# Kernel tuning notes

Measured on AMD Instinct MI355X. Metric: run time of the kernel, lower is better.

## Reference

```python
import itertools
import jax, jax.numpy as jnp
import numpy as np

B, S, D = 256, 49, 448          # batch, tokens (7x7), channels
H, KD, ED = 8, 32, 128          # heads, key_dim, expanded_key_dim (attn_ratio*key_dim)
QKV_OUT = H * (KD + KD + ED)    # 1536
MLP_HID = 4 * D                 # 1792
EPS = 1e-12
SCALE = KD ** -0.5


def _bias_idxs(resolution=7):
    points = list(itertools.product(range(resolution), range(resolution)))
    offsets, idxs = {}, []
    for p1 in points:
        for p2 in points:
            off = (abs(p1[0] - p2[0]), abs(p1[1] - p2[1]))
            if off not in offsets:
                offsets[off] = len(offsets)
            idxs.append(offsets[off])
    n = len(points)
    return np.asarray(idxs, np.int32).reshape(n, n), len(offsets)


def setup_inputs() -> dict:
    key = jax.random.key(0)
    ks = jax.random.split(key, 12)
    idxs_np, n_off = _bias_idxs(7)  # [49,49], 49 offsets
    s = 0.02
    return {
        "hidden_states": jax.random.normal(ks[0], (B, S, D), jnp.float32),
        "ln2_w": jnp.ones((D,), jnp.float32),
        "ln2_b": jnp.zeros((D,), jnp.float32),
        "qkv_w": jax.random.normal(ks[1], (QKV_OUT, D), jnp.float32) * s,
        "qkv_b": jnp.zeros((QKV_OUT,), jnp.float32),
        "proj_w": jax.random.normal(ks[2], (D, H * ED), jnp.float32) * s,
        "proj_b": jnp.zeros((D,), jnp.float32),
        "attention_biases": jax.random.normal(ks[3], (H, n_off), jnp.float32) * s,
        "fc1_w": jax.random.normal(ks[4], (MLP_HID, D), jnp.float32) * s,
        "fc1_b": jnp.zeros((MLP_HID,), jnp.float32),
        "fc2_w": jax.random.normal(ks[5], (D, MLP_HID), jnp.float32) * s,
        "fc2_b": jnp.zeros((D,), jnp.float32),
        "layer_scale_1": jnp.full((D,), 1e-5, jnp.float32),
        "layer_scale_2": jnp.full((D,), 1e-5, jnp.float32),
        "attention_bias_idxs": jnp.asarray(idxs_np),  # int32 [49,49]
    }


def _layernorm(x, w, b):
    mu = jnp.mean(x, axis=-1, keepdims=True)
    var = jnp.mean(jnp.square(x - mu), axis=-1, keepdims=True)
    return (x - mu) * jax.lax.rsqrt(var + EPS) * w + b


def reference(hidden_states, ln2_w, ln2_b, qkv_w, qkv_b, proj_w, proj_b,
              attention_biases, fc1_w, fc1_b, fc2_w, fc2_b,
              layer_scale_1, layer_scale_2, attention_bias_idxs):
    # NOTE: upstream code applies norm2 before BOTH attention and MLP (faithful).
    norm = _layernorm(hidden_states, ln2_w, ln2_b)  # [B,S,D]

    qkv = (norm @ qkv_w.T + qkv_b).reshape(B, S, H, KD + KD + ED)
    q, k, v = jnp.split(qkv, [KD, 2 * KD], axis=-1)  # [B,S,H,KD/KD/ED]

    bias = attention_biases[:, attention_bias_idxs]  # [H,S,S] gathered rel-pos bias
    scores = jnp.einsum("bqhd,bkhd->bhqk", q, k) * SCALE + bias[None]
    probs = jax.nn.softmax(scores, axis=-1)          # [B,H,S,S]

    ctx = jnp.einsum("bhqk,bkhd->bqhd", probs, v).reshape(B, S, H * ED)
    attn_out = ctx @ proj_w.T + proj_b               # [B,S,D]

    out = hidden_states + layer_scale_1 * attn_out
    mlp = jax.nn.gelu(norm @ fc1_w.T + fc1_b, approximate=False) @ fc2_w.T + fc2_b
    out = out + layer_scale_2 * mlp
    return out
```

## Files before the change

kernel.cpp:

```cpp
#include <hip/hip_runtime.h>
#include <hip/hip_bf16.h>
#include <cstdint>

#define B_    256
#define S_    49
#define D_    448
#define H_    8
#define NTOK  (B_*S_)
#define QKVO  1536
#define MLPH  1792
#define SCALE_ 0.17677669529663687f

using bf16x8  = __attribute__((ext_vector_type(8))) __bf16;
using ushort8 = __attribute__((ext_vector_type(8))) unsigned short;
using f32x4   = __attribute__((ext_vector_type(4))) float;

__device__ __forceinline__ unsigned short f2bf(float f){
  uint32_t u = __builtin_bit_cast(uint32_t, f);
  u += 0x7fffu + ((u >> 16) & 1u);
  return (unsigned short)(u >> 16);
}
__device__ __forceinline__ float b2f(unsigned short b){
  uint32_t u = ((uint32_t)b) << 16;
  return __builtin_bit_cast(float, u);
}

__device__ __forceinline__ void gload_lds16(const void* g, void* l){
  __builtin_amdgcn_global_load_lds(
      (const __attribute__((address_space(1))) void*)g,
      (__attribute__((address_space(3))) void*)l, 16, 0, 0);
}

#define P_S0 688128L
#define P_S1 1490944L
#define P_S2 1949696L
#define P_S3 2752512L
#define P_S4 2932736L
#define P_S5 2936064L
#define P_S6 2936576L
#define P_S7 2969344L
#define PREP_BLKS 6628
__global__ __launch_bounds__(448)
void prepln_k(const float* __restrict__ x, const float* __restrict__ lw,
              const float* __restrict__ lb, unsigned short* __restrict__ normb,
              const float* __restrict__ qkvw, const float* __restrict__ fc1w,
              const float* __restrict__ projw, const float* __restrict__ fc2w,
              const float* __restrict__ ls1, const float* __restrict__ ls2,
              const float* __restrict__ qkvb, const float* __restrict__ fc1b,
              const float* __restrict__ projb, const float* __restrict__ fc2b,
              const float* __restrict__ attb, const int* __restrict__ idxs,
              unsigned short* __restrict__ wcat, unsigned short* __restrict__ wfused,
              float* __restrict__ cbig, float* __restrict__ cbv,
              float* __restrict__ biasf){
  const int bid = blockIdx.x, t = threadIdx.x;
  if (bid < NTOK){
    const float v = x[(size_t)bid*448 + t];
    float s1 = v, s2 = v*v;
    #pragma unroll
    for (int o = 32; o; o >>= 1){ s1 += __shfl_xor(s1, o); s2 += __shfl_xor(s2, o); }
    __shared__ float a1[7], a2[7];
    const int wid = t >> 6;
    if ((t & 63) == 0){ a1[wid] = s1; a2[wid] = s2; }
    __syncthreads();
    float S1 = 0.f, S2 = 0.f;
    #pragma unroll
    for (int i = 0; i < 7; ++i){ S1 += a1[i]; S2 += a2[i]; }
    const float mu  = S1 * (1.f/448.f);
    const float var = S2 * (1.f/448.f) - mu*mu;
    const float rs  = rsqrtf(var + 1e-12f);
    normb[(size_t)bid*448 + t] = f2bf((v - mu)*rs*lw[t] + lb[t]);
  } else {
    const long i = (long)(bid - NTOK)*448 + t;
    if (i < P_S0){
      wcat[i] = f2bf(qkvw[i]);
    } else if (i < P_S1){
      long j = i - P_S0;
      wcat[i] = f2bf(fc1w[j]);
    } else if (i < P_S2){
      long j = i - P_S1;
      long r = j / 1024;
      wfused[r*2816 + (j - r*1024)] = f2bf(projw[j]*ls1[r]);
    } else if (i < P_S3){
      long j = i - P_S2;
      long r = j / 1792;
      wfused[r*2816 + 1024 + (j - r*1792)] = f2bf(fc2w[j]*ls2[r]);
    } else if (i < P_S4){
      long j = i - P_S3;
      wfused[448L*2816 + j] = 0;
    } else if (i < P_S5){
      long j = i - P_S4;
      cbig[j] = (j < 1536) ? qkvb[j] : fc1b[j - 1536];
    } else if (i < P_S6){
      long j = i - P_S5;
      cbv[j] = (j < 448) ? ls1[j]*projb[j] + ls2[j]*fc2b[j] : 0.f;
    } else if (i < P_S7){
      long j = i - P_S6;
      int h = (int)(j >> 12), r = (int)((j >> 6) & 63), c = (int)(j & 63);
      float v;
      if (c >= 49) v = -1e30f;
      else { int q = r < 49 ? r : 48; v = attb[h*49 + idxs[q*49 + c]]; }
      biasf[j] = v;
    }
  }
}

__global__ __launch_bounds__(256)
void gemm4_k(const unsigned short* __restrict__ A,
             const unsigned short* __restrict__ W,
             const float* __restrict__ bias,
             unsigned short* __restrict__ outB1,
             unsigned short* __restrict__ outB2,
             int splitBy, int nby)
{
  __shared__ char smem[65536];

  const int NB = gridDim.x;
  const int q8 = NB >> 3, r8 = NB & 7;
  const int xcd = blockIdx.x & 7, idx = blockIdx.x >> 3;
  const int wgid = (xcd < r8 ? xcd*(q8+1) : r8*(q8+1) + (xcd-r8)*q8) + idx;
  const int bx = wgid / nby, by = wgid - bx*nby;

  const int t = threadIdx.x, lane = t & 63, wid = t >> 6;
  const int wm = wid >> 1, wn = wid & 1;
  const int g = lane >> 4, li = lane & 15;
  f32x4 acc[4][4] = {};

  const int l3   = lane >> 3;
  const int sp   = (lane & 7) ^ l3;
  const int rofs = 2*l3 + (sp >> 2);
  const int cofs = (sp & 3)*8;

  auto stage = [&](int buf, int kt){
    char* Asb = smem + buf*16384;
    char* Bsb = Asb + 8192;
    const int k0 = kt*32;
    #pragma unroll
    for (int i = 0; i < 2; ++i){
      const int c = wid*2 + i;
      gload_lds16(A + (size_t)(bx*128 + c*16 + rofs)*448 + k0 + cofs, Asb + c*1024);
    }
    #pragma unroll
    for (int i = 0; i < 2; ++i){
      const int c = wid*2 + i;
      gload_lds16(W + (size_t)(by*128 + c*16 + rofs)*448 + k0 + cofs, Bsb + c*1024);
    }
  };

  const int sOff = (li >> 1)*128 + ((((li & 1)*4 + g) ^ (li >> 1)) << 4);

  stage(0, 0);
  stage(1, 1);
  int cur = 0, stg = 2;
  for (int kt = 0; kt < 14; ++kt){
    if (kt < 13) asm volatile("s_waitcnt vmcnt(4)" ::: "memory");
    else         asm volatile("s_waitcnt vmcnt(0)" ::: "memory");
    __builtin_amdgcn_s_barrier();
    if (kt + 2 < 14){ stage(stg, kt + 2); stg = (stg == 2) ? 0 : stg + 1; }
    char* Asb = smem + cur*16384;
    char* Bsb = Asb + 8192;
    bf16x8 af[4], bfr[4];
    #pragma unroll
    for (int mf = 0; mf < 4; ++mf)
      af[mf] = *reinterpret_cast<const bf16x8*>(Asb + (wm*4 + mf)*1024 + sOff);
    #pragma unroll
    for (int nf = 0; nf < 4; ++nf)
      bfr[nf] = *reinterpret_cast<const bf16x8*>(Bsb + (wn*4 + nf)*1024 + sOff);
    __builtin_amdgcn_s_setprio(1);
    #pragma unroll
    for (int mf = 0; mf < 4; ++mf)
      #pragma unroll
      for (int nf = 0; nf < 4; ++nf)
        acc[mf][nf] = __builtin_amdgcn_mfma_f32_16x16x32_bf16(af[mf], bfr[nf], acc[mf][nf], 0, 0, 0);
    __builtin_amdgcn_s_setprio(0);
    cur = (cur == 2) ? 0 : cur + 1;
  }
  __syncthreads();

  const bool dogelu = by >= splitBy;
  #pragma unroll
  for (int mf = 0; mf < 4; ++mf){
    #pragma unroll
    for (int nf = 0; nf < 4; ++nf){
      const int col = wn*64 + nf*16 + li;
      const float bi = bias[by*128 + col];
      #pragma unroll
      for (int j = 0; j < 4; ++j){
        const int row = wm*64 + mf*16 + g*4 + j;
        float v = acc[mf][nf][j] + bi;
        if (dogelu) v = 0.5f*v*(1.0f + erff(v*0.70710678118654752f));
        *reinterpret_cast<float*>(smem + row*512 + ((col*4) ^ (((row >> 2) & 3) << 6))) = v;
      }
    }
  }
  __syncthreads();
  const int lr = lane >> 4, lc = lane & 15;
  #pragma unroll
  for (int it = 0; it < 8; ++it){
    const int r = wid*32 + it*4 + lr;
    const int sw = ((r >> 2) & 3) << 6;
    const f32x4 v0 = *reinterpret_cast<const f32x4*>(smem + r*512 + ((lc*32)      ^ sw));
    const f32x4 v1 = *reinterpret_cast<const f32x4*>(smem + r*512 + ((lc*32 + 16) ^ sw));
    ushort8 u;
    #pragma unroll
    for (int k = 0; k < 4; ++k){ u[k] = f2bf(v0[k]); u[4+k] = f2bf(v1[k]); }
    const int grow = bx*128 + r;
    if (by < splitBy)
      *reinterpret_cast<ushort8*>(outB1 + (size_t)grow*QKVO + by*128 + lc*8) = u;
    else
      *reinterpret_cast<ushort8*>(outB2 + (size_t)grow*MLPH + (by - splitBy)*128 + lc*8) = u;
  }
}

__global__ __launch_bounds__(256)
void gemm1_k(const unsigned short* __restrict__ A1, int lda1, int nkt1,
             const unsigned short* __restrict__ A2, int lda2, int nkt,
             const unsigned short* __restrict__ W, int ldw,
             const float* __restrict__ bias,
             const float* __restrict__ resid, float* __restrict__ outF,
             int nby)
{
  constexpr int BN = 64, NF = 2;
  __shared__ char smem[49152];

  const int NB = gridDim.x;
  const int q8 = NB >> 3, r8 = NB & 7;
  const int xcd = blockIdx.x & 7, idx = blockIdx.x >> 3;
  const int wgid = (xcd < r8 ? xcd*(q8+1) : r8*(q8+1) + (xcd-r8)*q8) + idx;
  const int bx = wgid / nby, by = wgid - bx*nby;

  const int t = threadIdx.x, lane = t & 63, wid = t >> 6;
  const int wm = wid >> 1, wn = wid & 1;
  const int g = lane >> 4, li = lane & 15;
  f32x4 acc[4][NF] = {};

  const int srow  = lane >> 3;
  const int scolw = ((lane & 7) ^ srow) * 8;

  auto stage = [&](int buf, int kt){
    char* Asb = smem + buf*16384;
    char* Bsb = smem + 32768 + buf*(BN*128);
    const unsigned short* Ab; int lda, k0;
    if (kt < nkt1){ Ab = A1; lda = lda1; k0 = kt*64; }
    else          { Ab = A2; lda = lda2; k0 = (kt - nkt1)*64; }
    #pragma unroll
    for (int i = 0; i < 4; ++i){
      const int c = wid*4 + i;
      gload_lds16(Ab + (size_t)(bx*128 + c*8 + srow)*lda + k0 + scolw,
                  Asb + c*1024);
    }
    #pragma unroll
    for (int i = 0; i < NF; ++i){
      const int c = wid*NF + i;
      gload_lds16(W + (size_t)(by*BN + c*8 + srow)*ldw + kt*64 + scolw,
                  Bsb + c*1024);
    }
  };

  int buf = 0;
  stage(0, 0);
  for (int kt = 0; kt < nkt; ++kt){
    __syncthreads();
    if (kt + 1 < nkt) stage(buf ^ 1, kt + 1);
    char* Asb = smem + buf*16384;
    char* Bsb = smem + 32768 + buf*(BN*128);
    #pragma unroll
    for (int ks = 0; ks < 2; ++ks){
      const int kk2 = (ks*32 + g*8)*2;
      bf16x8 af[4], bfr[NF];
      #pragma unroll
      for (int mf = 0; mf < 4; ++mf){
        const int row = wm*64 + mf*16 + li;
        af[mf] = *reinterpret_cast<const bf16x8*>(
            Asb + row*128 + (kk2 ^ ((row & 7) << 4)));
      }
      #pragma unroll
      for (int nf = 0; nf < NF; ++nf){
        const int row = wn*(BN/2) + nf*16 + li;
        bfr[nf] = *reinterpret_cast<const bf16x8*>(
            Bsb + row*128 + (kk2 ^ ((row & 7) << 4)));
      }
      #pragma unroll
      for (int mf = 0; mf < 4; ++mf)
        #pragma unroll
        for (int nf = 0; nf < NF; ++nf)
          acc[mf][nf] = __builtin_amdgcn_mfma_f32_16x16x32_bf16(af[mf], bfr[nf], acc[mf][nf], 0, 0, 0);
    }
    buf ^= 1;
  }
  __syncthreads();

  const int lr = lane >> 4, lc = lane & 15;
  #pragma unroll
  for (int mf = 0; mf < 4; ++mf){
    #pragma unroll
    for (int nf = 0; nf < NF; ++nf){
      const int col = wn*32 + nf*16 + li;
      const float bi = bias[by*64 + col];
      #pragma unroll
      for (int j = 0; j < 4; ++j){
        const int rt = wm*64 + mf*16 + g*4 + j;
        *reinterpret_cast<float*>(smem + rt*256 + ((col*4) ^ (((rt >> 2) & 1) << 6)))
            = acc[mf][nf][j] + bi;
      }
    }
  }
  __syncthreads();
  #pragma unroll
  for (int i = 0; i < 8; ++i){
    const int r = wid*32 + i*4 + lr;
    const int sw = ((r >> 2) & 1) << 6;
    const f32x4 v = *reinterpret_cast<const f32x4*>(smem + r*256 + ((lc*16) ^ sw));
    const size_t o = (size_t)(bx*128 + r)*448 + by*64 + lc*4;
    const f32x4 rs = *reinterpret_cast<const f32x4*>(resid + o);
    *reinterpret_cast<f32x4*>(outF + o) = rs + v;
  }
}

__global__ __launch_bounds__(256)
void attn_mfma_k(const unsigned short* __restrict__ qkv,
                 const float* __restrict__ biasf,
                 unsigned short* __restrict__ ctx)
{
  const int bh = blockIdx.x;
  const int b = bh >> 3, h = bh & 7;
  __shared__ unsigned short QKs[64*64];
  __shared__ unsigned short Vs[64*128];
  __shared__ unsigned short Ps[64*64];
  const int t = threadIdx.x, lane = t & 63, w = t >> 6;
  const int g = lane >> 4, li = lane & 15;
  const size_t qbase = ((size_t)b*49)*QKVO + (size_t)h*192;

  {
    const int kk = lane >> 3, ss = lane & 7;
    #pragma unroll
    for (int i = 0; i < 2; ++i){
      const int kb = (w*2 + i)*8;
      const int k  = kb + kk;
      const int ks = k < 49 ? k : 48;
      gload_lds16(qkv + qbase + (size_t)ks*QKVO + ((ss ^ (k & 7))*8),
                  (char*)QKs + kb*128);
    }
    const int kv = lane >> 4, sv = lane & 15;
    #pragma unroll
    for (int i = 0; i < 4; ++i){
      const int kb = (w*4 + i)*4;
      const int k  = kb + kv;
      const int ks = k < 49 ? k : 48;
      const int swz = (((unsigned)k >> 3) & 3) << 1;
      gload_lds16(qkv + qbase + 64 + (size_t)ks*QKVO + ((sv ^ swz)*8),
                  (char*)Vs + kb*256);
    }
  }
  asm volatile("s_waitcnt vmcnt(0)" ::: "memory");
  for (int e = t; e < 15*8; e += 256){
    const int k = 49 + (e >> 3), s = e & 7;
    *reinterpret_cast<bf16x8*>((char*)QKs + k*128 + s*16) = (bf16x8){};
  }
  for (int e = t; e < 15*16; e += 256){
    const int k = 49 + (e >> 4), s = e & 15;
    *reinterpret_cast<bf16x8*>((char*)Vs + k*256 + s*16) = (bf16x8){};
  }
  __syncthreads();

  const int qrow = w*16 + li;
  const bf16x8 afq = *reinterpret_cast<const bf16x8*>(
      (char*)QKs + qrow*128 + ((g ^ (qrow & 7)) << 4));
  f32x4 accs[4];
  #pragma unroll
  for (int nf = 0; nf < 4; ++nf){
    const int krow = nf*16 + li;
    const bf16x8 bfr = *reinterpret_cast<const bf16x8*>(
        (char*)QKs + krow*128 + (((4 + g) ^ (krow & 7)) << 4));
    f32x4 z = {};
    accs[nf] = __builtin_amdgcn_mfma_f32_16x16x32_bf16(afq, bfr, z, 0, 0, 0);
  }

  #pragma unroll
  for (int j = 0; j < 4; ++j){
    const int row = w*16 + g*4 + j;
    float sv[4];
    #pragma unroll
    for (int nf = 0; nf < 4; ++nf)
      sv[nf] = accs[nf][j]*SCALE_ + biasf[h*4096 + row*64 + nf*16 + li];
    float m = fmaxf(fmaxf(sv[0], sv[1]), fmaxf(sv[2], sv[3]));
    #pragma unroll
    for (int o = 8; o; o >>= 1) m = fmaxf(m, __shfl_xor(m, o));
    float e[4], s = 0.f;
    #pragma unroll
    for (int nf = 0; nf < 4; ++nf){ e[nf] = __expf(sv[nf] - m); s += e[nf]; }
    #pragma unroll
    for (int o = 8; o; o >>= 1) s += __shfl_xor(s, o);
    const float inv = 1.f / s;
    #pragma unroll
    for (int nf = 0; nf < 4; ++nf){
      const int byte = (row*128 + (nf*16 + li)*2) ^ ((row & 7) << 4);
      *reinterpret_cast<unsigned short*>((char*)Ps + byte) = f2bf(e[nf]*inv);
    }
  }
  __syncthreads();

  f32x4 accp[4][2] = {};
  #pragma unroll
  for (int kt = 0; kt < 2; ++kt){
    bf16x8 pa[4];
    #pragma unroll
    for (int mt = 0; mt < 4; ++mt){
      const int q = mt*16 + li;
      const int byte = (q*128 + kt*64 + g*16) ^ ((q & 7) << 4);
      pa[mt] = *reinterpret_cast<const bf16x8*>((char*)Ps + byte);
    }
    #pragma unroll
    for (int nf = 0; nf < 2; ++nf){
      const int d = w*32 + nf*16 + li;
      ushort8 vbu;
      #pragma unroll
      for (int j = 0; j < 8; ++j){
        const int k = kt*32 + g*8 + j;
        const int byte = (k*256 + d*2) ^ ((((unsigned)k >> 3) & 3) << 5);
        vbu[j] = *reinterpret_cast<const unsigned short*>((char*)Vs + byte);
      }
      const bf16x8 vb = __builtin_bit_cast(bf16x8, vbu);
      #pragma unroll
      for (int mt = 0; mt < 4; ++mt)
        accp[mt][nf] = __builtin_amdgcn_mfma_f32_16x16x32_bf16(pa[mt], vb, accp[mt][nf], 0, 0, 0);
    }
  }

  const size_t obase = ((size_t)b*49)*1024 + (size_t)h*128;
  #pragma unroll
  for (int mt = 0; mt < 4; ++mt){
    #pragma unroll
    for (int nf = 0; nf < 2; ++nf){
      #pragma unroll
      for (int j = 0; j < 4; ++j){
        const int row = mt*16 + g*4 + j;
        if (row < 49){
          const int col = w*32 + nf*16 + li;
          ctx[obase + (size_t)row*1024 + col] = f2bf(accp[mt][nf][j]);
        }
      }
    }
  }
}

extern "C" void kernel_launch(void* const* d_in, const int* in_sizes, int n_in,
                              void* d_out, int out_size, void* d_ws, size_t ws_size,
                              hipStream_t stream)
{
  const float* hidden = (const float*)d_in[0];
  const float* ln2w   = (const float*)d_in[1];
  const float* ln2b   = (const float*)d_in[2];
  const float* qkvw   = (const float*)d_in[3];
  const float* qkvb   = (const float*)d_in[4];
  const float* projw  = (const float*)d_in[5];
  const float* projb  = (const float*)d_in[6];
  const float* attb   = (const float*)d_in[7];
  const float* fc1w   = (const float*)d_in[8];
  const float* fc1b   = (const float*)d_in[9];
  const float* fc2w   = (const float*)d_in[10];
  const float* fc2b   = (const float*)d_in[11];
  const float* ls1    = (const float*)d_in[12];
  const float* ls2    = (const float*)d_in[13];
  const int*   aidx   = (const int*)d_in[14];
  float* out = (float*)d_out;

  char* p = (char*)d_ws;
  auto alloc = [&](size_t bytes){ void* r = (void*)p; p += (bytes + 255) & ~(size_t)255; return r; };
  unsigned short* wcat   = (unsigned short*)alloc((size_t)3328*448*2);
  unsigned short* wfused = (unsigned short*)alloc((size_t)512*2816*2);
  unsigned short* normb  = (unsigned short*)alloc((size_t)NTOK*448*2);
  unsigned short* qkvv   = (unsigned short*)alloc((size_t)NTOK*QKVO*2);
  unsigned short* ctx    = (unsigned short*)alloc((size_t)NTOK*1024*2);
  unsigned short* hid    = (unsigned short*)alloc((size_t)NTOK*MLPH*2);
  float*          biasf  = (float*)alloc((size_t)8*64*64*4);
  float*          cbig   = (float*)alloc((size_t)3328*4);
  float*          cbv    = (float*)alloc((size_t)512*4);

  prepln_k<<<NTOK + PREP_BLKS, 448, 0, stream>>>(hidden, ln2w, ln2b, normb,
                                                 qkvw, fc1w, projw, fc2w, ls1, ls2,
                                                 qkvb, fc1b, projb, fc2b, attb, aidx,
                                                 wcat, wfused, cbig, cbv, biasf);

  gemm4_k<<<98*26, 256, 0, stream>>>(normb, wcat, cbig, qkvv, hid, 12, 26);
  attn_mfma_k<<<B_*H_, 256, 0, stream>>>(qkvv, biasf, ctx);
  gemm1_k<<<98*7, 256, 0, stream>>>(ctx, 1024, 16, hid, MLPH, 44,
                                    wfused, 2816, cbv,
                                    hidden, out, 7);
}
```

Before: 150.6 us.

## Triple-buffer gemm1 LDS pipeline with vmcnt waits and MFMA priority boost

Changes the gemm1 kernel from double to triple buffering in LDS, keeping two K-tiles of loads in flight. A per-iteration __syncthreads is replaced by an explicit s_waitcnt vmcnt plus s_barrier. It also raises wave priority around the MFMA block. The goal is to hide global-to-LDS latency better, at the cost of 72KB of LDS per block, which may reduce occupancy. The single barrier per iteration before restaging a buffer relies on the 3-buffer rotation to avoid overwriting data still being read.

```diff
diff --git a/kernel.cpp b/kernel.cpp
--- a/kernel.cpp
+++ b/kernel.cpp
@@ -219,8 +219,7 @@
              const float* __restrict__ resid, float* __restrict__ outF,
              int nby)
 {
-  constexpr int BN = 64, NF = 2;
-  __shared__ char smem[49152];
+  __shared__ char smem[73728];
 
   const int NB = gridDim.x;
   const int q8 = NB >> 3, r8 = NB & 7;
@@ -231,14 +230,14 @@
   const int t = threadIdx.x, lane = t & 63, wid = t >> 6;
   const int wm = wid >> 1, wn = wid & 1;
   const int g = lane >> 4, li = lane & 15;
-  f32x4 acc[4][NF] = {};
+  f32x4 acc[4][2] = {};
 
   const int srow  = lane >> 3;
   const int scolw = ((lane & 7) ^ srow) * 8;
 
   auto stage = [&](int buf, int kt){
     char* Asb = smem + buf*16384;
-    char* Bsb = smem + 32768 + buf*(BN*128);
+    char* Bsb = smem + 49152 + buf*8192;
     const unsigned short* Ab; int lda, k0;
     if (kt < nkt1){ Ab = A1; lda = lda1; k0 = kt*64; }
     else          { Ab = A2; lda = lda2; k0 = (kt - nkt1)*64; }
@@ -249,24 +248,27 @@
                   Asb + c*1024);
     }
     #pragma unroll
-    for (int i = 0; i < NF; ++i){
-      const int c = wid*NF + i;
-      gload_lds16(W + (size_t)(by*BN + c*8 + srow)*ldw + kt*64 + scolw,
+    for (int i = 0; i < 2; ++i){
+      const int c = wid*2 + i;
+      gload_lds16(W + (size_t)(by*64 + c*8 + srow)*ldw + kt*64 + scolw,
                   Bsb + c*1024);
     }
   };
 
-  int buf = 0;
   stage(0, 0);
+  stage(1, 1);
+  int cur = 0, stg = 2;
   for (int kt = 0; kt < nkt; ++kt){
-    __syncthreads();
-    if (kt + 1 < nkt) stage(buf ^ 1, kt + 1);
-    char* Asb = smem + buf*16384;
-    char* Bsb = smem + 32768 + buf*(BN*128);
+    if (kt < nkt - 1) asm volatile("s_waitcnt vmcnt(6)" ::: "memory");
+    else              asm volatile("s_waitcnt vmcnt(0)" ::: "memory");
+    __builtin_amdgcn_s_barrier();
+    if (kt + 2 < nkt){ stage(stg, kt + 2); stg = (stg == 2) ? 0 : stg + 1; }
+    char* Asb = smem + cur*16384;
+    char* Bsb = smem + 49152 + cur*8192;
     #pragma unroll
     for (int ks = 0; ks < 2; ++ks){
       const int kk2 = (ks*32 + g*8)*2;
-      bf16x8 af[4], bfr[NF];
+      bf16x8 af[4], bfr[2];
       #pragma unroll
       for (int mf = 0; mf < 4; ++mf){
         const int row = wm*64 + mf*16 + li;
@@ -274,18 +276,20 @@
             Asb + row*128 + (kk2 ^ ((row & 7) << 4)));
       }
       #pragma unroll
-      for (int nf = 0; nf < NF; ++nf){
-        const int row = wn*(BN/2) + nf*16 + li;
+      for (int nf = 0; nf < 2; ++nf){
+        const int row = wn*32 + nf*16 + li;
         bfr[nf] = *reinterpret_cast<const bf16x8*>(
             Bsb + row*128 + (kk2 ^ ((row & 7) << 4)));
       }
+      __builtin_amdgcn_s_setprio(1);
       #pragma unroll
       for (int mf = 0; mf < 4; ++mf)
         #pragma unroll
-        for (int nf = 0; nf < NF; ++nf)
+        for (int nf = 0; nf < 2; ++nf)
           acc[mf][nf] = __builtin_amdgcn_mfma_f32_16x16x32_bf16(af[mf], bfr[nf], acc[mf][nf], 0, 0, 0);
-    }
-    buf ^= 1;
+      __builtin_amdgcn_s_setprio(0);
+    }
+    cur = (cur == 2) ? 0 : cur + 1;
   }
   __syncthreads();
 
@@ -293,7 +297,7 @@
   #pragma unroll
   for (int mf = 0; mf < 4; ++mf){
     #pragma unroll
-    for (int nf = 0; nf < NF; ++nf){
+    for (int nf = 0; nf < 2; ++nf){
       const int col = wn*32 + nf*16 + li;
       const float bi = bias[by*64 + col];
       #pragma unroll
```

After: 160.8 us. +6.8%, slower.
